# Performance work log

Hardware: AMD Instinct MI355X
Metric: run time of the kernel (lower is better)

Reference implementation:

```python
import jax, jax.numpy as jnp
import numpy as np

FILTERS = 64
NBITS = 4
NUE = 4
NSPU = 2
NST = NUE * NSPU           # 8 streams total
OUT_CH = NST * NBITS       # 32 output channels
NBS, NANT = 1, 16
CIN = NBS * NANT * 2 + NBS * NANT * NUE * NSPU * 2 + NUE * NSPU + 1  # 297


def hard_sigmoid(x):
    # Keras ConvLSTM2D default recurrent_activation
    return jnp.clip(0.2 * x + 0.5, 0.0, 1.0)


def conv2d(x, w):
    # x: [N,H,W,C], w: [kh,kw,Cin,Cout], SAME padding
    return jax.lax.conv_general_dilated(x, w, (1, 1), 'SAME',
                                        dimension_numbers=('NHWC', 'HWIO', 'NHWC'))


def convlstm2d(x, Wx, Wh, b):
    """Keras ConvLSTM2D (return_sequences=True), gate order i,f,c,o.
    x: [B,T,H,W,Cin] -> [B,T,H,W,F].
    Input-to-hidden convs are precomputed for all timesteps at once;
    only the cheap hidden-to-hidden conv is inside the scan."""
    B, T, H, W, Cin = x.shape
    F = Wh.shape[2]
    xz = conv2d(x.reshape(B * T, H, W, Cin), Wx).reshape(B, T, H, W, 4 * F) + b
    xz = jnp.moveaxis(xz, 1, 0)  # [T,B,H,W,4F]
    h0 = jnp.zeros((B, H, W, F), x.dtype)

    def step(carry, z_in):
        h, c = carry
        z = z_in + conv2d(h, Wh)
        zi, zf, zg, zo = jnp.split(z, 4, axis=-1)
        i = hard_sigmoid(zi)
        f = hard_sigmoid(zf)
        g = jnp.tanh(zg)
        o = hard_sigmoid(zo)
        c = f * c + i * g
        h = o * jnp.tanh(c)
        return (h, c), h

    _, hs = jax.lax.scan(step, (h0, h0), xz)
    return jnp.moveaxis(hs, 0, 1)  # [B,T,H,W,F]


def _lstm_params(key, cin, f, scale=0.05):
    k1, k2, k3 = jax.random.split(key, 3)
    Wx = jax.random.normal(k1, (3, 3, cin, 4 * f), jnp.float32) * scale
    Wh = jax.random.normal(k2, (3, 3, f, 4 * f), jnp.float32) * scale
    b = jax.random.normal(k3, (4 * f,), jnp.float32) * scale
    return Wx, Wh, b


def setup_inputs() -> dict:
    key = jax.random.key(0)
    ks = jax.random.split(key, 10)
    B, T, W = 2, 14, 1536
    inp = {
        'y_ri': jax.random.normal(ks[0], (B, NBS, NANT, T, W, 2), jnp.float32),
        'h_ri': jax.random.normal(ks[1], (B, NBS, NANT, NUE, NSPU, T, W, 2), jnp.float32),
        'err_var': jax.random.uniform(ks[2], (1, 1, 1, NUE, NSPU, T, W), jnp.float32),
        'no': jax.random.uniform(ks[3], (1,), jnp.float32),
    }
    inp['Wx_in'], inp['Wh_in'], inp['b_in'] = _lstm_params(ks[4], CIN, FILTERS)
    inp['Wx_r0'], inp['Wh_r0'], inp['b_r0'] = _lstm_params(ks[5], FILTERS, FILTERS)
    inp['Wx_r1'], inp['Wh_r1'], inp['b_r1'] = _lstm_params(ks[6], FILTERS, FILTERS)
    inp['Wx_out'], inp['Wh_out'], inp['b_out'] = _lstm_params(ks[7], FILTERS, OUT_CH)
    return inp


def _forward(y_ri, h_ri, err_var, no,
             Wx_in, Wh_in, b_in,
             Wx_r0, Wh_r0, b_r0,
             Wx_r1, Wh_r1, b_r1,
             Wx_out, Wh_out, b_out):
    B, nbs, nant, T, W, _ = y_ri.shape
    # y: [B,nbs,nant,T,W,2] -> [B,T,W,nbs*nant*2]
    y_feats = jnp.transpose(y_ri, (0, 3, 4, 1, 2, 5)).reshape(B, T, W, -1)
    # h: [B,nbs,nant,ue,spu,T,W,2] -> [B,T,W,nbs*nant*ue*spu*2]
    h_feats = jnp.transpose(h_ri, (0, 5, 6, 1, 2, 3, 4, 7)).reshape(B, T, W, -1)
    # err_var: [1,1,1,ue,spu,T,W] -> [B,T,W,ue*spu]
    ev = jnp.transpose(err_var[0, 0, 0], (2, 3, 0, 1)).reshape(1, T, W, NUE * NSPU)
    err_feats = jnp.broadcast_to(ev, (B, T, W, NUE * NSPU))
    no_feat = jnp.broadcast_to(no.reshape(1, 1, 1, 1), (B, T, W, 1))
    z = jnp.concatenate([y_feats, h_feats, err_feats, no_feat], axis=-1)
    z = z[:, :, :, None, :]  # [B,T,W,1,C]

    z = convlstm2d(z, Wx_in, Wh_in, b_in)
    # residual blocks (in_ch == filters, so identity skip)
    z = convlstm2d(z, Wx_r0, Wh_r0, b_r0) + z
    z = convlstm2d(z, Wx_r1, Wh_r1, b_r1) + z
    z = convlstm2d(z, Wx_out, Wh_out, b_out)

    z = z[:, :, :, 0, :]  # [B,T,W,OUT_CH]
    N = T * W
    z = z.reshape(B, N, NUE, NSPU, NBITS)
    z = jnp.transpose(z, (0, 2, 3, 1, 4))
    return z.reshape(B, NUE, NSPU, N * NBITS)


def reference(y_ri, h_ri, err_var, no,
              Wx_in, Wh_in, b_in,
              Wx_r0, Wh_r0, b_r0,
              Wx_r1, Wh_r1, b_r1,
              Wx_out, Wh_out, b_out):
    return _forward(y_ri, h_ri, err_var, no,
                    Wx_in, Wh_in, b_in,
                    Wx_r0, Wh_r0, b_r0,
                    Wx_r1, Wh_r1, b_r1,
                    Wx_out, Wh_out, b_out)
```

## Files before the change

### kernel.cpp

```cpp
#include <hip/hip_runtime.h>
#include <hip/hip_bf16.h>


#define BB   2
#define TT   14
#define LL   1536
#define CINR 297
#define CP_IN 320
#define NSTRIP 96
#define NBLK  (BB * NSTRIP)
#define WIN  48

typedef __attribute__((ext_vector_type(8))) short short8;
typedef __attribute__((ext_vector_type(4))) float floatx4;

static constexpr size_t U_WBIN_HI  = 0;
static constexpr size_t U_WBIN_LO  = 245760;
static constexpr size_t U_WBR0_HI  = 491520;
static constexpr size_t U_WBR0_LO  = 540672;
static constexpr size_t U_WBR1_HI  = 589824;
static constexpr size_t U_WBR1_LO  = 638976;
static constexpr size_t U_WBOUT_HI = 688128;
static constexpr size_t U_WBOUT_LO = 712704;
static constexpr size_t U_WHTIN    = 737280;
static constexpr size_t U_WHTR0    = 786432;
static constexpr size_t U_WHTR1    = 835584;
static constexpr size_t U_WHTOUT   = 884736;
static constexpr size_t OFF_BIN   = 448512;
static constexpr size_t OFF_BR0   = 448768;
static constexpr size_t OFF_BR1   = 449024;
static constexpr size_t OFF_BOUT  = 449280;
static constexpr size_t OFF_Z0HI  = 458752;
static constexpr size_t SZ_Z0PL   = 6881280;
static constexpr size_t OFF_Z0LO  = OFF_Z0HI + SZ_Z0PL;
static constexpr size_t OFF_XZ    = OFF_Z0LO + SZ_Z0PL;
static constexpr size_t SZ_XZ     = (size_t)BB*TT*LL*256;
static constexpr size_t OFF_SEQ   = OFF_Z0HI;
static constexpr size_t OFF_SEQHI = OFF_SEQ + (size_t)BB*TT*LL*64;
static constexpr size_t OFF_SEQLO = OFF_SEQHI + (size_t)BB*TT*LL*32;

__device__ __forceinline__ float hsig(float x) {
    return fminf(fmaxf(0.2f * x + 0.5f, 0.0f), 1.0f);
}
__device__ __forceinline__ float ftanh(float x) {
    float e = __expf(2.0f * x);
    return 1.0f - 2.0f / (e + 1.0f);
}
__device__ __forceinline__ unsigned short f2bf(float x) {
    unsigned int u = __builtin_bit_cast(unsigned int, x);
    u += 0x7fffu + ((u >> 16) & 1u);
    return (unsigned short)(u >> 16);
}
__device__ __forceinline__ float bf2f(unsigned short h) {
    unsigned int u = ((unsigned int)h) << 16;
    return __builtin_bit_cast(float, u);
}

__global__ __launch_bounds__(256)
void prep_weights_kernel(const float* wx_in, const float* wh_in, const float* b_in,
                         const float* wx_r0, const float* wh_r0, const float* b_r0,
                         const float* wx_r1, const float* wh_r1, const float* b_r1,
                         const float* wx_out, const float* wh_out, const float* b_out,
                         float* __restrict__ ws)
{
    int idx = blockIdx.x * 256 + threadIdx.x;
    unsigned short* u = (unsigned short*)ws;
    if (idx < 245760) {
        int n = idx / 960, k = idx % 960;
        int kh = k / CP_IN, ci = k % CP_IN;
        float v = 0.0f;
        if (ci < CINR) {
            int f = n >> 2, g = n & 3;
            v = wx_in[((size_t)(kh * 3 + 1) * CINR + ci) * 256 + g * 64 + f];
        }
        unsigned short hi = f2bf(v);
        u[U_WBIN_HI + idx] = hi;
        u[U_WBIN_LO + idx] = f2bf(v - bf2f(hi));
        return;
    }
    idx -= 245760;
    if (idx < 49152) {
        int n = idx / 192, k = idx % 192;
        int kh = k >> 6, ci = k & 63;
        int f = n >> 2, g = n & 3;
        float v = wx_r0[((size_t)(kh * 3 + 1) * 64 + ci) * 256 + g * 64 + f];
        unsigned short hi = f2bf(v);
        u[U_WBR0_HI + idx] = hi;
        u[U_WBR0_LO + idx] = f2bf(v - bf2f(hi));
        return;
    }
    idx -= 49152;
    if (idx < 49152) {
        int n = idx / 192, k = idx % 192;
        int kh = k >> 6, ci = k & 63;
        int f = n >> 2, g = n & 3;
        float v = wx_r1[((size_t)(kh * 3 + 1) * 64 + ci) * 256 + g * 64 + f];
        unsigned short hi = f2bf(v);
        u[U_WBR1_HI + idx] = hi;
        u[U_WBR1_LO + idx] = f2bf(v - bf2f(hi));
        return;
    }
    idx -= 49152;
    if (idx < 24576) {
        int n = idx / 192, k = idx % 192;
        int kh = k >> 6, ci = k & 63;
        int f = n >> 2, g = n & 3;
        float v = wx_out[((size_t)(kh * 3 + 1) * 64 + ci) * 128 + g * 32 + f];
        unsigned short hi = f2bf(v);
        u[U_WBOUT_HI + idx] = hi;
        u[U_WBOUT_LO + idx] = f2bf(v - bf2f(hi));
        return;
    }
    idx -= 24576;
    if (idx < 49152) {
        int n = idx / 192, k = idx % 192, kh = k >> 6, ci = k & 63;
        u[U_WHTIN + idx] = f2bf(wh_in[((size_t)(kh * 3 + 1) * 64 + ci) * 256 + n]);
        return;
    }
    idx -= 49152;
    if (idx < 49152) {
        int n = idx / 192, k = idx % 192, kh = k >> 6, ci = k & 63;
        u[U_WHTR0 + idx] = f2bf(wh_r0[((size_t)(kh * 3 + 1) * 64 + ci) * 256 + n]);
        return;
    }
    idx -= 49152;
    if (idx < 49152) {
        int n = idx / 192, k = idx % 192, kh = k >> 6, ci = k & 63;
        u[U_WHTR1 + idx] = f2bf(wh_r1[((size_t)(kh * 3 + 1) * 64 + ci) * 256 + n]);
        return;
    }
    idx -= 49152;
    if (idx < 12288) {
        int n = idx / 96, k = idx % 96, kh = k / 32, ci = k % 32;
        u[U_WHTOUT + idx] = f2bf(wh_out[((size_t)(kh * 3 + 1) * 32 + ci) * 128 + n]);
        return;
    }
    idx -= 12288;
    if (idx < 256) { int f = idx >> 2, g = idx & 3; ws[OFF_BIN + idx] = b_in[g * 64 + f]; return; }
    idx -= 256;
    if (idx < 256) { int f = idx >> 2, g = idx & 3; ws[OFF_BR0 + idx] = b_r0[g * 64 + f]; return; }
    idx -= 256;
    if (idx < 256) { int f = idx >> 2, g = idx & 3; ws[OFF_BR1 + idx] = b_r1[g * 64 + f]; return; }
    idx -= 256;
    if (idx < 128) { int f = idx >> 2, g = idx & 3; ws[OFF_BOUT + idx] = b_out[g * 32 + f]; return; }
}

__global__ __launch_bounds__(256)
void build_features_kernel(const float* __restrict__ y,
                           const float* __restrict__ h,
                           const float* __restrict__ ev,
                           const float* __restrict__ no,
                           unsigned short* __restrict__ z0hi,
                           unsigned short* __restrict__ z0lo)
{
    long long idx = (long long)blockIdx.x * 256 + threadIdx.x;
    const long long total = (long long)BB * TT * LL * CP_IN;
    if (idx >= total) return;
    int c = (int)(idx % CP_IN);
    long long rest = idx / CP_IN;
    int l = (int)(rest % LL); rest /= LL;
    int t = (int)(rest % TT);
    int b = (int)(rest / TT);
    float v = 0.0f;
    if (c < 32) {
        int na = c >> 1, ri = c & 1;
        v = y[((((long long)b * 16 + na) * TT + t) * LL + l) * 2 + ri];
    } else if (c < 288) {
        int q = c - 32;
        int ri = q & 1, nspu = (q >> 1) & 1, nue = (q >> 2) & 3, na = q >> 4;
        v = h[((((((long long)b * 16 + na) * 4 + nue) * 2 + nspu) * TT + t) * LL + l) * 2 + ri];
    } else if (c < 296) {
        int q = c - 288; int nspu = q & 1, nue = q >> 1;
        v = ev[(((long long)(nue * 2 + nspu) * TT + t) * LL) + l];
    } else if (c == 296) {
        v = no[0];
    }
    unsigned short hi = f2bf(v);
    z0hi[idx] = hi;
    z0lo[idx] = f2bf(v - bf2f(hi));
}

__global__ __launch_bounds__(256)
void xz_gemm_mfma_kernel(const unsigned short* __restrict__ Ahi,
                         const unsigned short* __restrict__ Alo,
                         int Cpitch,
                         const unsigned short* __restrict__ Bhi,
                         const unsigned short* __restrict__ Blo,
                         const float* __restrict__ bias,
                         float* __restrict__ out, int Ncol)
{
    __shared__ unsigned short AsHi[66 * 40], AsLo[66 * 40];
    __shared__ unsigned short WsHi[3 * 64 * 40], WsLo[3 * 64 * 40];
    const int tid  = threadIdx.x;
    const int lane = tid & 63;
    const int wv   = tid >> 6;
    const int m    = lane & 15;
    const int quad = lane >> 4;
    const int bt   = blockIdx.y;
    const int l0   = blockIdx.x * 64;
    const int n0   = blockIdx.z * 64;
    const int K    = 3 * Cpitch;
    const int NC   = Cpitch >> 5;

    floatx4 acc[4];
#pragma unroll
    for (int i = 0; i < 4; i++) acc[i] = (floatx4){0.f, 0.f, 0.f, 0.f};

    for (int cc = 0; cc < NC; ++cc) {
        __syncthreads();
        for (int i = tid; i < 66 * 4; i += 256) {
            int r = i >> 2, c8 = (i & 3) * 8;
            int row = l0 + r - 1;
            short8 vh = (short8)0, vl = (short8)0;
            if (row >= 0 && row < LL) {
                size_t off = ((size_t)bt * LL + row) * Cpitch + cc * 32 + c8;
                vh = *reinterpret_cast<const short8*>(&Ahi[off]);
                vl = *reinterpret_cast<const short8*>(&Alo[off]);
            }
            *reinterpret_cast<short8*>(&AsHi[r * 40 + c8]) = vh;
            *reinterpret_cast<short8*>(&AsLo[r * 40 + c8]) = vl;
        }
        for (int i = tid; i < 3 * 64 * 4; i += 256) {
            int kh = i >> 8;
            int r2 = i & 255;
            int n = r2 >> 2, c8 = (r2 & 3) * 8;
            size_t off = (size_t)(n0 + n) * K + kh * Cpitch + cc * 32 + c8;
            *reinterpret_cast<short8*>(&WsHi[(kh * 64 + n) * 40 + c8]) =
                *reinterpret_cast<const short8*>(&Bhi[off]);
            *reinterpret_cast<short8*>(&WsLo[(kh * 64 + n) * 40 + c8]) =
                *reinterpret_cast<const short8*>(&Blo[off]);
        }
        __syncthreads();
#pragma unroll
        for (int kh = 0; kh < 3; ++kh) {
            const int bofs = (kh * 64 + wv * 16 + m) * 40 + quad * 8;
            const short8 bh = *reinterpret_cast<const short8*>(&WsHi[bofs]);
            const short8 bl = *reinterpret_cast<const short8*>(&WsLo[bofs]);
#pragma unroll
            for (int mt = 0; mt < 4; ++mt) {
                const int aofs = (mt * 16 + m + kh) * 40 + quad * 8;
                const short8 ah = *reinterpret_cast<const short8*>(&AsHi[aofs]);
                const short8 al = *reinterpret_cast<const short8*>(&AsLo[aofs]);
                acc[mt] = __builtin_amdgcn_mfma_f32_16x16x32_bf16(al, bh, acc[mt], 0, 0, 0);
                acc[mt] = __builtin_amdgcn_mfma_f32_16x16x32_bf16(ah, bl, acc[mt], 0, 0, 0);
                acc[mt] = __builtin_amdgcn_mfma_f32_16x16x32_bf16(ah, bh, acc[mt], 0, 0, 0);
            }
        }
    }
    const int col = n0 + wv * 16 + m;
    const float bv = bias[col];
#pragma unroll
    for (int mt = 0; mt < 4; ++mt) {
#pragma unroll
        for (int reg = 0; reg < 4; ++reg) {
            int l = l0 + mt * 16 + quad * 4 + reg;
            out[((size_t)bt * LL + l) * Ncol + col] = acc[mt][reg] + bv;
        }
    }
}

template <int F_, bool RESID, bool OUTW>
__global__ __launch_bounds__(64 * (F_ / 16))
void lstm_scan_kernel(const float* __restrict__ xz,
                      const unsigned short* __restrict__ WhT,
                      float* seq,
                      unsigned short* __restrict__ seqhb,
                      unsigned short* __restrict__ seqlb,
                      float* __restrict__ dout)
{
    constexpr int NW = F_ / 16;
    constexpr int NT = 64 * NW;
    constexpr int K  = 3 * F_;
    constexpr int KS = K / 32;
    constexpr int KH = KS / 3;
    constexpr int HP = F_ + 8;
    __shared__ unsigned short Hs[2][(WIN + 2) * HP];

    const int tid  = threadIdx.x;
    const int lane = tid & 63;
    const int wv   = tid >> 6;
    const int m    = lane & 15;
    const int quad = lane >> 4;
    const int blk  = blockIdx.x;
    const int b    = blk / NSTRIP;
    const int o0   = (blk % NSTRIP) * 16;
    const int f    = wv * 16 + m;

    short8 bfr[4][KS];
#pragma unroll
    for (int g = 0; g < 4; g++)
#pragma unroll
        for (int ks = 0; ks < KS; ks++) {
            const int n  = g * F_ + f;
            const int k0 = ks * 32 + quad * 8;
            bfr[g][ks] = *reinterpret_cast<const short8*>(&WhT[(size_t)n * K + k0]);
        }

    for (int idx = tid; idx < (WIN + 2) * HP; idx += NT) {
        Hs[0][idx] = 0; Hs[1][idx] = 0;
    }
    __syncthreads();

    float c[3][4];
#pragma unroll
    for (int i = 0; i < 3; i++)
#pragma unroll
        for (int j = 0; j < 4; j++) c[i][j] = 0.0f;

    int cur = 0;
    for (int t = 0; t < TT; ++t) {
        const size_t btL = ((size_t)b * TT + t) * LL;

        float4 xzv[3][4];
        float  rsv[4];
#pragma unroll
        for (int mt = 0; mt < 3; ++mt)
#pragma unroll
            for (int reg = 0; reg < 4; ++reg) {
                const int w = mt * 16 + quad * 4 + reg;
                const int l = o0 - 16 + w;
                float4 v = make_float4(0.f, 0.f, 0.f, 0.f);
                if (l >= 0 && l < LL && w >= t && w < WIN - t)
                    v = *reinterpret_cast<const float4*>(
                        &xz[(btL + l) * (size_t)(4 * F_) + f * 4]);
                xzv[mt][reg] = v;
            }
        if (RESID) {
#pragma unroll
            for (int reg = 0; reg < 4; ++reg) {
                const int l = o0 + quad * 4 + reg;
                rsv[reg] = seq[(btL + l) * F_ + f];
            }
        }

        const int nxt = cur ^ 1;
#pragma unroll
        for (int mt = 0; mt < 3; ++mt) {
            floatx4 zi = {0.f, 0.f, 0.f, 0.f};
            floatx4 zf = {0.f, 0.f, 0.f, 0.f};
            floatx4 zg = {0.f, 0.f, 0.f, 0.f};
            floatx4 zo = {0.f, 0.f, 0.f, 0.f};
            if (t > 0) {
#pragma unroll
                for (int kh = 0; kh < 3; kh++) {
#pragma unroll
                    for (int hf = 0; hf < KH; hf++) {
                        const short8 af = *reinterpret_cast<const short8*>(
                            &Hs[cur][(mt * 16 + m + kh) * HP + hf * 32 + quad * 8]);
                        const int ks = kh * KH + hf;
                        zi = __builtin_amdgcn_mfma_f32_16x16x32_bf16(af, bfr[0][ks], zi, 0, 0, 0);
                        zf = __builtin_amdgcn_mfma_f32_16x16x32_bf16(af, bfr[1][ks], zf, 0, 0, 0);
                        zg = __builtin_amdgcn_mfma_f32_16x16x32_bf16(af, bfr[2][ks], zg, 0, 0, 0);
                        zo = __builtin_amdgcn_mfma_f32_16x16x32_bf16(af, bfr[3][ks], zo, 0, 0, 0);
                    }
                }
            }
#pragma unroll
            for (int reg = 0; reg < 4; ++reg) {
                const int w = mt * 16 + quad * 4 + reg;
                const int l = o0 - 16 + w;
                const bool valid = (l >= 0 && l < LL);
                const float4 z4 = xzv[mt][reg];
                const float ig = hsig(z4.x + zi[reg]);
                const float fg = hsig(z4.y + zf[reg]);
                const float gg = ftanh(z4.z + zg[reg]);
                const float og = hsig(z4.w + zo[reg]);
                float cn = fg * c[mt][reg] + ig * gg;
                float hn = og * ftanh(cn);
                if (!valid) { cn = 0.0f; hn = 0.0f; }
                c[mt][reg] = cn;
                Hs[nxt][(1 + w) * HP + f] = f2bf(hn);
                if (w >= 16 && w < 32) {
                    if (OUTW) {
                        const int ue = f >> 3, spu = (f >> 2) & 1, bit = f & 3;
                        const size_t n = (size_t)t * LL + l;
                        dout[(((size_t)b * 4 + ue) * 2 + spu) * ((size_t)TT * LL * 4)
                             + n * 4 + bit] = hn;
                    } else {
                        float v = hn;
                        if (RESID) v += rsv[reg];
                        seq[(btL + l) * F_ + f] = v;
                        const unsigned short hi = f2bf(v);
                        seqhb[(btL + l) * F_ + f] = hi;
                        seqlb[(btL + l) * F_ + f] = f2bf(v - bf2f(hi));
                    }
                }
            }
        }
        __syncthreads();
        cur = nxt;
    }
}

extern "C" void kernel_launch(void* const* d_in, const int* in_sizes, int n_in,
                              void* d_out, int out_size, void* d_ws, size_t ws_size,
                              hipStream_t stream)
{
    (void)in_sizes; (void)n_in; (void)out_size; (void)ws_size;
    const float* y_ri   = (const float*)d_in[0];
    const float* h_ri   = (const float*)d_in[1];
    const float* evar   = (const float*)d_in[2];
    const float* no     = (const float*)d_in[3];
    const float* wx_in  = (const float*)d_in[4];
    const float* wh_in  = (const float*)d_in[5];
    const float* b_in   = (const float*)d_in[6];
    const float* wx_r0  = (const float*)d_in[7];
    const float* wh_r0  = (const float*)d_in[8];
    const float* b_r0   = (const float*)d_in[9];
    const float* wx_r1  = (const float*)d_in[10];
    const float* wh_r1  = (const float*)d_in[11];
    const float* b_r1   = (const float*)d_in[12];
    const float* wx_out = (const float*)d_in[13];
    const float* wh_out = (const float*)d_in[14];
    const float* b_out  = (const float*)d_in[15];

    float* ws = (float*)d_ws;
    unsigned short* wu = (unsigned short*)d_ws;
    float* dout = (float*)d_out;

    prep_weights_kernel<<<2068, 256, 0, stream>>>(
        wx_in, wh_in, b_in, wx_r0, wh_r0, b_r0,
        wx_r1, wh_r1, b_r1, wx_out, wh_out, b_out, ws);
    {
        long long total = (long long)BB * TT * LL * CP_IN;
        int blocks = (int)((total + 255) / 256);
        build_features_kernel<<<blocks, 256, 0, stream>>>(
            y_ri, h_ri, evar, no,
            (unsigned short*)(ws + OFF_Z0HI), (unsigned short*)(ws + OFF_Z0LO));
    }

    float* xz    = ws + OFF_XZ;
    float* seq   = ws + OFF_SEQ;
    unsigned short* seqhb = (unsigned short*)(ws + OFF_SEQHI);
    unsigned short* seqlb = (unsigned short*)(ws + OFF_SEQLO);

    const dim3 gIn(LL / 64, BB * TT, 4);
    const dim3 gO (LL / 64, BB * TT, 2);

    xz_gemm_mfma_kernel<<<gIn, 256, 0, stream>>>(
        (unsigned short*)(ws + OFF_Z0HI), (unsigned short*)(ws + OFF_Z0LO), CP_IN,
        wu + U_WBIN_HI, wu + U_WBIN_LO, ws + OFF_BIN, xz, 256);
    lstm_scan_kernel<64, false, false><<<NBLK, 256, 0, stream>>>(
        xz, wu + U_WHTIN, seq, seqhb, seqlb, nullptr);

    xz_gemm_mfma_kernel<<<gIn, 256, 0, stream>>>(
        seqhb, seqlb, 64, wu + U_WBR0_HI, wu + U_WBR0_LO, ws + OFF_BR0, xz, 256);
    lstm_scan_kernel<64, true, false><<<NBLK, 256, 0, stream>>>(
        xz, wu + U_WHTR0, seq, seqhb, seqlb, nullptr);

    xz_gemm_mfma_kernel<<<gIn, 256, 0, stream>>>(
        seqhb, seqlb, 64, wu + U_WBR1_HI, wu + U_WBR1_LO, ws + OFF_BR1, xz, 256);
    lstm_scan_kernel<64, true, false><<<NBLK, 256, 0, stream>>>(
        xz, wu + U_WHTR1, seq, seqhb, seqlb, nullptr);

    xz_gemm_mfma_kernel<<<gO, 256, 0, stream>>>(
        seqhb, seqlb, 64, wu + U_WBOUT_HI, wu + U_WBOUT_LO, ws + OFF_BOUT, xz, 128);
    lstm_scan_kernel<32, false, true><<<NBLK, 128, 0, stream>>>(
        xz, wu + U_WHTOUT, nullptr, nullptr, nullptr, dout);
}
```

Measured before the change: 517.4 us.

## Widen xz GEMM tile to 128 columns and prefetch next K-chunk into registers

The input-projection GEMM kernel now computes 128 output columns per block instead of 64, so each wave keeps two accumulator sets and each staged A tile is reused across twice as many columns. The grid's z dimension is halved to match. Global loads for the next 32-channel chunk are issued into registers before the MFMA loop runs, overlapping memory latency with compute. This raises register and LDS use per block and halves the block count, which may reduce occupancy and parallelism.

```diff
diff --git a/kernel.cpp b/kernel.cpp
--- a/kernel.cpp
+++ b/kernel.cpp
@@ -190,7 +190,7 @@
                          float* __restrict__ out, int Ncol)
 {
     __shared__ unsigned short AsHi[66 * 40], AsLo[66 * 40];
-    __shared__ unsigned short WsHi[3 * 64 * 40], WsLo[3 * 64 * 40];
+    __shared__ unsigned short WsHi[3 * 128 * 40], WsLo[3 * 128 * 40];
     const int tid  = threadIdx.x;
     const int lane = tid & 63;
     const int wv   = tid >> 6;
@@ -198,63 +198,126 @@
     const int quad = lane >> 4;
     const int bt   = blockIdx.y;
     const int l0   = blockIdx.x * 64;
-    const int n0   = blockIdx.z * 64;
+    const int n0   = blockIdx.z * 128;
     const int K    = 3 * Cpitch;
     const int NC   = Cpitch >> 5;
 
-    floatx4 acc[4];
-#pragma unroll
-    for (int i = 0; i < 4; i++) acc[i] = (floatx4){0.f, 0.f, 0.f, 0.f};
+    const int aC8   = (tid & 3) * 8;
+    const int aRow  = (tid >> 5) * 8 + ((tid >> 2) & 3) * 2 + ((tid >> 4) & 1);
+    const int aRowT = 64 + ((tid >> 2) & 1);
+
+    int wRow[6], wKh[6], wNn[6];
+#pragma unroll
+    for (int k = 0; k < 6; ++k) {
+        const int s = tid + k * 256;
+        const int r = (s >> 5) * 8 + ((s >> 2) & 3) * 2 + ((s >> 4) & 1);
+        wRow[k] = r; wKh[k] = r >> 7; wNn[k] = r & 127;
+    }
+
+    short8 aH0 = (short8)0, aL0 = (short8)0, aH1 = (short8)0, aL1 = (short8)0;
+    short8 wH[6], wL[6];
+
+    {
+        const int row = l0 + aRow - 1;
+        if (row >= 0 && row < LL) {
+            size_t off = ((size_t)bt * LL + row) * Cpitch + aC8;
+            aH0 = *reinterpret_cast<const short8*>(&Ahi[off]);
+            aL0 = *reinterpret_cast<const short8*>(&Alo[off]);
+        }
+        if (tid < 8) {
+            const int rowt = l0 + aRowT - 1;
+            if (rowt >= 0 && rowt < LL) {
+                size_t off = ((size_t)bt * LL + rowt) * Cpitch + aC8;
+                aH1 = *reinterpret_cast<const short8*>(&Ahi[off]);
+                aL1 = *reinterpret_cast<const short8*>(&Alo[off]);
+            }
+        }
+#pragma unroll
+        for (int k = 0; k < 6; ++k) {
+            size_t off = (size_t)(n0 + wNn[k]) * K + (size_t)wKh[k] * Cpitch + aC8;
+            wH[k] = *reinterpret_cast<const short8*>(&Bhi[off]);
+            wL[k] = *reinterpret_cast<const short8*>(&Blo[off]);
+        }
+    }
+
+    floatx4 acc[4][2];
+#pragma unroll
+    for (int i = 0; i < 4; i++)
+#pragma unroll
+        for (int j = 0; j < 2; j++) acc[i][j] = (floatx4){0.f, 0.f, 0.f, 0.f};
 
     for (int cc = 0; cc < NC; ++cc) {
         __syncthreads();
-        for (int i = tid; i < 66 * 4; i += 256) {
-            int r = i >> 2, c8 = (i & 3) * 8;
-            int row = l0 + r - 1;
-            short8 vh = (short8)0, vl = (short8)0;
+        *reinterpret_cast<short8*>(&AsHi[aRow * 40 + aC8]) = aH0;
+        *reinterpret_cast<short8*>(&AsLo[aRow * 40 + aC8]) = aL0;
+        if (tid < 8) {
+            *reinterpret_cast<short8*>(&AsHi[aRowT * 40 + aC8]) = aH1;
+            *reinterpret_cast<short8*>(&AsLo[aRowT * 40 + aC8]) = aL1;
+        }
+#pragma unroll
+        for (int k = 0; k < 6; ++k) {
+            *reinterpret_cast<short8*>(&WsHi[wRow[k] * 40 + aC8]) = wH[k];
+            *reinterpret_cast<short8*>(&WsLo[wRow[k] * 40 + aC8]) = wL[k];
+        }
+        if (cc + 1 < NC) {
+            const int c32 = (cc + 1) * 32;
+            const int row = l0 + aRow - 1;
+            aH0 = (short8)0; aL0 = (short8)0;
             if (row >= 0 && row < LL) {
-                size_t off = ((size_t)bt * LL + row) * Cpitch + cc * 32 + c8;
-                vh = *reinterpret_cast<const short8*>(&Ahi[off]);
-                vl = *reinterpret_cast<const short8*>(&Alo[off]);
-            }
-            *reinterpret_cast<short8*>(&AsHi[r * 40 + c8]) = vh;
-            *reinterpret_cast<short8*>(&AsLo[r * 40 + c8]) = vl;
-        }
-        for (int i = tid; i < 3 * 64 * 4; i += 256) {
-            int kh = i >> 8;
-            int r2 = i & 255;
-            int n = r2 >> 2, c8 = (r2 & 3) * 8;
-            size_t off = (size_t)(n0 + n) * K + kh * Cpitch + cc * 32 + c8;
-            *reinterpret_cast<short8*>(&WsHi[(kh * 64 + n) * 40 + c8]) =
-                *reinterpret_cast<const short8*>(&Bhi[off]);
-            *reinterpret_cast<short8*>(&WsLo[(kh * 64 + n) * 40 + c8]) =
-                *reinterpret_cast<const short8*>(&Blo[off]);
+                size_t off = ((size_t)bt * LL + row) * Cpitch + c32 + aC8;
+                aH0 = *reinterpret_cast<const short8*>(&Ahi[off]);
+                aL0 = *reinterpret_cast<const short8*>(&Alo[off]);
+            }
+            if (tid < 8) {
+                aH1 = (short8)0; aL1 = (short8)0;
+                const int rowt = l0 + aRowT - 1;
+                if (rowt >= 0 && rowt < LL) {
+                    size_t off = ((size_t)bt * LL + rowt) * Cpitch + c32 + aC8;
+                    aH1 = *reinterpret_cast<const short8*>(&Ahi[off]);
+                    aL1 = *reinterpret_cast<const short8*>(&Alo[off]);
+                }
+            }
+#pragma unroll
+            for (int k = 0; k < 6; ++k) {
+                size_t off = (size_t)(n0 + wNn[k]) * K + (size_t)wKh[k] * Cpitch + c32 + aC8;
+                wH[k] = *reinterpret_cast<const short8*>(&Bhi[off]);
+                wL[k] = *reinterpret_cast<const short8*>(&Blo[off]);
+            }
         }
         __syncthreads();
 #pragma unroll
         for (int kh = 0; kh < 3; ++kh) {
-            const int bofs = (kh * 64 + wv * 16 + m) * 40 + quad * 8;
-            const short8 bh = *reinterpret_cast<const short8*>(&WsHi[bofs]);
-            const short8 bl = *reinterpret_cast<const short8*>(&WsLo[bofs]);
+            const int b0 = (kh * 128 + wv * 16 + m) * 40 + quad * 8;
+            const int b1 = (kh * 128 + 64 + wv * 16 + m) * 40 + quad * 8;
+            const short8 bh0 = *reinterpret_cast<const short8*>(&WsHi[b0]);
+            const short8 bl0 = *reinterpret_cast<const short8*>(&WsLo[b0]);
+            const short8 bh1 = *reinterpret_cast<const short8*>(&WsHi[b1]);
+            const short8 bl1 = *reinterpret_cast<const short8*>(&WsLo[b1]);
 #pragma unroll
             for (int mt = 0; mt < 4; ++mt) {
                 const int aofs = (mt * 16 + m + kh) * 40 + quad * 8;
                 const short8 ah = *reinterpret_cast<const short8*>(&AsHi[aofs]);
                 const short8 al = *reinterpret_cast<const short8*>(&AsLo[aofs]);
-                acc[mt] = __builtin_amdgcn_mfma_f32_16x16x32_bf16(al, bh, acc[mt], 0, 0, 0);
-                acc[mt] = __builtin_amdgcn_mfma_f32_16x16x32_bf16(ah, bl, acc[mt], 0, 0, 0);
-                acc[mt] = __builtin_amdgcn_mfma_f32_16x16x32_bf16(ah, bh, acc[mt], 0, 0, 0);
-            }
-        }
-    }
-    const int col = n0 + wv * 16 + m;
-    const float bv = bias[col];
-#pragma unroll
-    for (int mt = 0; mt < 4; ++mt) {
-#pragma unroll
-        for (int reg = 0; reg < 4; ++reg) {
-            int l = l0 + mt * 16 + quad * 4 + reg;
-            out[((size_t)bt * LL + l) * Ncol + col] = acc[mt][reg] + bv;
+                acc[mt][0] = __builtin_amdgcn_mfma_f32_16x16x32_bf16(al, bh0, acc[mt][0], 0, 0, 0);
+                acc[mt][0] = __builtin_amdgcn_mfma_f32_16x16x32_bf16(ah, bl0, acc[mt][0], 0, 0, 0);
+                acc[mt][0] = __builtin_amdgcn_mfma_f32_16x16x32_bf16(ah, bh0, acc[mt][0], 0, 0, 0);
+                acc[mt][1] = __builtin_amdgcn_mfma_f32_16x16x32_bf16(al, bh1, acc[mt][1], 0, 0, 0);
+                acc[mt][1] = __builtin_amdgcn_mfma_f32_16x16x32_bf16(ah, bl1, acc[mt][1], 0, 0, 0);
+                acc[mt][1] = __builtin_amdgcn_mfma_f32_16x16x32_bf16(ah, bh1, acc[mt][1], 0, 0, 0);
+            }
+        }
+    }
+#pragma unroll
+    for (int nt = 0; nt < 2; ++nt) {
+        const int col = n0 + nt * 64 + wv * 16 + m;
+        const float bv = bias[col];
+#pragma unroll
+        for (int mt = 0; mt < 4; ++mt) {
+#pragma unroll
+            for (int reg = 0; reg < 4; ++reg) {
+                int l = l0 + mt * 16 + quad * 4 + reg;
+                out[((size_t)bt * LL + l) * Ncol + col] = acc[mt][nt][reg] + bv;
+            }
         }
     }
 }
@@ -434,8 +497,8 @@
     unsigned short* seqhb = (unsigned short*)(ws + OFF_SEQHI);
     unsigned short* seqlb = (unsigned short*)(ws + OFF_SEQLO);
 
-    const dim3 gIn(LL / 64, BB * TT, 4);
-    const dim3 gO (LL / 64, BB * TT, 2);
+    const dim3 gIn(LL / 64, BB * TT, 2);
+    const dim3 gO (LL / 64, BB * TT, 1);
 
     xz_gemm_mfma_kernel<<<gIn, 256, 0, stream>>>(
         (unsigned short*)(ws + OFF_Z0HI), (unsigned short*)(ws + OFF_Z0LO), CP_IN,
```

Measured after the change: 502.3 us. 1.03x faster.
